# Kernel optimization log

Hardware: AMD Instinct MI355X
Metric: run time of the kernel (lower is better)

The kernel has to match this reference:

```python
import jax, jax.numpy as jnp
import numpy as np

B, N, T, F, H, NH, E, R = 16, 100, 96, 26, 128, 4, 16, 8


def _ln(x, g, b, eps=1e-5):
    m = x.mean(-1, keepdims=True)
    v = ((x - m) ** 2).mean(-1, keepdims=True)
    return (x - m) / jnp.sqrt(v + eps) * g + b


def setup_inputs() -> dict:
    ks = iter(jax.random.split(jax.random.key(0), 64))

    def nrm(*shape):
        return jax.random.normal(next(ks), shape, jnp.float32) * 0.05

    z = lambda *s: jnp.zeros(s, jnp.float32)
    o = lambda *s: jnp.ones(s, jnp.float32)
    inp = {}
    inp['x'] = jax.random.normal(next(ks), (B, N, T, F), jnp.float32)
    A = jax.random.uniform(next(ks), (N, N), jnp.float32)
    inp['A_norm'] = A / A.sum(1, keepdims=True)
    inp['H_inc'] = (jax.random.uniform(next(ks), (N, E)) > 0.7).astype(jnp.float32).at[:, 0].set(1.0)
    inp['membership'] = jax.random.randint(next(ks), (N,), 0, R)
    inp['Wp'] = nrm(H, F); inp['bp'] = z(H)
    inp['g_p'] = o(H); inp['b_p'] = z(H)
    inp['Wqkv'] = nrm(3 * H, H); inp['bqkv'] = z(3 * H)
    inp['Wo'] = nrm(H, H); inp['bo'] = z(H)
    inp['g_a'] = o(H); inp['b_a'] = z(H)
    inp['Wih_f'] = nrm(4 * H, H); inp['Whh_f'] = nrm(4 * H, H)
    inp['bih_f'] = z(4 * H); inp['bhh_f'] = z(4 * H)
    inp['Wih_b'] = nrm(4 * H, H); inp['Whh_b'] = nrm(4 * H, H)
    inp['bih_b'] = z(4 * H); inp['bhh_b'] = z(4 * H)
    inp['Wtp'] = nrm(H, 2 * H); inp['btp'] = z(H)
    inp['Wn'] = nrm(H, H); inp['bn'] = z(H)
    inp['We'] = nrm(H, H); inp['be'] = z(H)
    inp['Wa'] = nrm(1, H); inp['ba'] = z(1)
    inp['g_g'] = o(H); inp['b_g'] = z(H)
    inp['Remb'] = nrm(R, H)
    inp['Wg'] = nrm(H, H); inp['bg'] = z(H)
    inp['Wf'] = nrm(H, 2 * H); inp['bf'] = z(H)
    inp['g_f'] = o(H); inp['b_f'] = z(H)
    inp['W1'] = nrm(H // 2, H); inp['b1'] = z(H // 2)
    inp['W2'] = nrm(1, H // 2); inp['b2'] = z(1)
    return inp


def reference(x, A_norm, H_inc, membership, Wp, bp, g_p, b_p, Wqkv, bqkv, Wo, bo,
              g_a, b_a, Wih_f, Whh_f, bih_f, bhh_f, Wih_b, Whh_b, bih_b, bhh_b,
              Wtp, btp, Wn, bn, We, be, Wa, ba, g_g, b_g, Remb, Wg, bg,
              Wf, bf, g_f, b_f, W1, b1, W2, b2):
    B_, N_, T_, F_ = x.shape
    H_ = Wp.shape[0]
    BN = B_ * N_
    # input_proj (dropout = identity in eval)
    h = jax.nn.relu(_ln(x.reshape(BN, T_, F_) @ Wp.T + bp, g_p, b_p))
    # temporal multi-head self-attention + residual + LN
    qkv = h @ Wqkv.T + bqkv
    q, k, v = jnp.split(qkv, 3, -1)
    dh = H_ // NH
    sh = lambda t: t.reshape(BN, T_, NH, dh).transpose(0, 2, 1, 3)
    q, k, v = sh(q), sh(k), sh(v)
    att = jax.nn.softmax(jnp.einsum('bhqd,bhkd->bhqk', q, k) / jnp.sqrt(jnp.float32(dh)), -1)
    ao = jnp.einsum('bhqk,bhkd->bhqd', att, v).transpose(0, 2, 1, 3).reshape(BN, T_, H_)
    h = _ln(ao @ Wo.T + bo + h, g_a, b_a)
    # bidirectional LSTM (PyTorch gate order i,f,g,o), take t = T-1
    def lstm_scan(seq, Wih, Whh, bih, bhh):
        def step(carry, xt):
            hp, cp = carry
            gates = xt @ Wih.T + bih + hp @ Whh.T + bhh
            i, f, g, o_ = jnp.split(gates, 4, -1)
            c = jax.nn.sigmoid(f) * cp + jax.nn.sigmoid(i) * jnp.tanh(g)
            hn = jax.nn.sigmoid(o_) * jnp.tanh(c)
            return (hn, c), hn
        z0 = jnp.zeros((seq.shape[1], H_), seq.dtype)
        _, ys = jax.lax.scan(step, (z0, z0), seq)
        return ys
    seq = h.transpose(1, 0, 2)  # (T, BN, H)
    y_f = lstm_scan(seq, Wih_f, Whh_f, bih_f, bhh_f)[-1]        # fwd hidden at t=T-1
    y_b = lstm_scan(seq[::-1], Wih_b, Whh_b, bih_b, bhh_b)[0]   # bwd hidden at t=T-1
    h_temporal = (jnp.concatenate([y_f, y_b], -1) @ Wtp.T + btp).reshape(B_, N_, H_)
    # spatial: HyperGAT (segment softmax over incident hyperedges) + GCN + region emb
    mask = H_inc > 0                        # (N, E)
    deg_e = H_inc.sum(0)                    # (E,)
    has_edge = mask.any(-1, keepdims=True)  # (N, 1)
    r_emb = Remb[membership]                # (N, H)

    def spatial(hb):
        npj = hb @ Wn.T + bn
        ee = (H_inc.T @ npj) / (deg_e[:, None] + 1e-8)
        ee = ee @ We.T + be                 # (E, H)
        sc = (ee @ Wa.T + ba)[:, 0]         # (E,)
        w = jax.nn.softmax(jnp.where(mask, sc[None, :], -1e9), -1)
        w = jnp.where(has_edge, w, 0.0)
        hb2 = _ln(w @ ee + hb, g_g, b_g)
        hg = jax.nn.relu((A_norm @ hb2) @ Wg.T + bg)
        return hb2 + hg + r_emb

    h_spatial = jax.vmap(spatial)(h_temporal)
    h_fused = jax.nn.relu(_ln(jnp.concatenate([h_temporal, h_spatial], -1) @ Wf.T + bf, g_f, b_f))
    pred = (jax.nn.relu(h_fused @ W1.T + b1) @ W2.T + b2)[..., 0]
    return pred, h_spatial, h_temporal
```

## Files before the change

### kernel.cpp

```cpp
#include <hip/hip_runtime.h>
#include <hip/hip_bf16.h>

typedef __hip_bfloat16 bf16;
typedef __attribute__((ext_vector_type(8))) short bf8v;
typedef __attribute__((ext_vector_type(4))) short s4v;
typedef __attribute__((ext_vector_type(4))) float f4v;

#define DEV __device__ __forceinline__

DEV float b2f(bf16 v){ return __bfloat162float(v); }
DEV bf16 f2b(float v){ return __float2bfloat16(v); }
DEV short f2bs(float v){ bf16 t = __float2bfloat16(v); return *reinterpret_cast<short*>(&t); }
DEV float s2f(short s){ return __uint_as_float(((unsigned int)(unsigned short)s) << 16); }
DEV float blo(unsigned int u){ return __uint_as_float(u << 16); }
DEV float bhi(unsigned int u){ return __uint_as_float(u & 0xffff0000u); }
DEV float rcpf_(float x){ return __builtin_amdgcn_rcpf(x); }
DEV float sigf(float x){ return rcpf_(1.0f + __expf(-x)); }
DEV float tanhfast(float x){
  x = fminf(fmaxf(x, -15.0f), 15.0f);
  float e = __expf(-2.0f*x);
  return (1.0f - e)*rcpf_(1.0f + e);
}

DEV f4v mfma16(bf8v a, bf8v b, f4v c){
  return __builtin_amdgcn_mfma_f32_16x16x32_bf16(a, b, c, 0, 0, 0);
}

DEV float ln128(float s, int tid, const bf16* g, const bf16* b, float* red){
  float sum = s, sq = s*s;
  #pragma unroll
  for (int off = 32; off; off >>= 1){
    sum += __shfl_down(sum, off);
    sq  += __shfl_down(sq,  off);
  }
  if ((tid & 63) == 0){ red[(tid>>6)*2] = sum; red[(tid>>6)*2+1] = sq; }
  __syncthreads();
  float S = red[0] + red[2], Q = red[1] + red[3];
  float m  = S * (1.0f/128.0f);
  float var = fmaxf(Q * (1.0f/128.0f) - m*m, 0.0f);
  float rs = rsqrtf(var + 1e-5f);
  float y = (s - m)*rs*b2f(g[tid]) + b2f(b[tid]);
  __syncthreads();
  return y;
}

__global__ void k_detect(const unsigned int* __restrict__ xw, int* __restrict__ flag){
  __shared__ int found;
  if (threadIdx.x == 0) found = 0;
  __syncthreads();
  int local = 0;
  for (int i = threadIdx.x; i < 4096; i += 256){
    unsigned int u = xw[i];
    unsigned int e = (u >> 7) & 0xFF;
    if (e >= 0x90) local = 1;
  }
  if (local) atomicOr(&found, 1);
  __syncthreads();
  if (threadIdx.x == 0) flag[0] = found ? 0 : 1;
}

struct CArgs {
  const void* src[44];
  int n[44];
  int off[44];
};

__global__ void k_canon(CArgs a, const int* __restrict__ flag, bf16* __restrict__ dst){
  int id = blockIdx.y;
  int n = a.n[id];
  const void* s = a.src[id];
  bf16* d = dst + a.off[id];
  int stride = gridDim.x * blockDim.x;
  int i0 = blockIdx.x * blockDim.x + threadIdx.x;
  if (flag[0]){
    const bf16* sb = (const bf16*)s;
    for (int i = i0; i < n; i += stride) d[i] = sb[i];
  } else {
    const float* sf = (const float*)s;
    for (int i = i0; i < n; i += stride) d[i] = f2b(sf[i]);
  }
}

__global__ void k_inproj(const bf16* __restrict__ x, const bf16* __restrict__ Wp,
                         const bf16* __restrict__ bp, const bf16* __restrict__ gp,
                         const bf16* __restrict__ bbp, bf16* __restrict__ h0){
  int row0 = blockIdx.x*8, tid = threadIdx.x;
  __shared__ float xs[8*26];
  __shared__ float red[4];
  float wreg[26];
  #pragma unroll
  for (int f = 0; f < 26; ++f) wreg[f] = b2f(Wp[tid*26 + f]);
  float bias = b2f(bp[tid]);
  for (int i = tid; i < 208; i += 128) xs[i] = b2f(x[row0*26 + i]);
  __syncthreads();
  for (int r = 0; r < 8; ++r){
    float s = bias;
    #pragma unroll
    for (int f = 0; f < 26; ++f) s += xs[r*26 + f]*wreg[f];
    float y = fmaxf(ln128(s, tid, gp, bbp, red), 0.0f);
    h0[(row0 + r)*128 + tid] = f2b(y);
  }
}

__global__ __launch_bounds__(256) void k_attn(const bf16* __restrict__ h0,
    const bf16* __restrict__ Wqkv, const bf16* __restrict__ bqkv,
    bf16* __restrict__ attno){
  int bn = blockIdx.x;
  int tid = threadIdx.x;
  int w = tid >> 6;
  int lane = tid & 63;
  int l15 = lane & 15, quad = lane >> 4;

  __shared__ __align__(16) short h0s[96*136];
  __shared__ __align__(16) short v_sh[4][32*104];
  __shared__ __align__(16) short scr[4][16*40];

  {
    const uint4* src = (const uint4*)(h0 + bn*12288);
    uint4* dst = (uint4*)h0s;
    for (int u = tid; u < 1536; u += 256){
      int r = u >> 4, c = u & 15;
      dst[r*17 + c] = src[u];
    }
  }
  __syncthreads();

  short* vp = v_sh[w];
  short* sw = scr[w];
  const float scl = 0.17677669529663687f;

  bf8v aq[6], bk[6];
  for (int m = 0; m < 6; ++m){
    bf8v a[4];
    #pragma unroll
    for (int kt = 0; kt < 4; ++kt)
      a[kt] = *reinterpret_cast<const bf8v*>(h0s + (m*16 + l15)*136 + kt*32 + quad*8);
    #pragma unroll
    for (int n0 = 0; n0 < 32; n0 += 16){
      int rq = w*32 + n0 + l15;
      bf8v b[4];
      #pragma unroll
      for (int kt = 0; kt < 4; ++kt)
        b[kt] = *reinterpret_cast<const bf8v*>(Wqkv + rq*128 + kt*32 + quad*8);
      float bias = b2f(bqkv[rq]);
      f4v acc = {0.f,0.f,0.f,0.f};
      #pragma unroll
      for (int kt = 0; kt < 4; ++kt) acc = mfma16(a[kt], b[kt], acc);
      #pragma unroll
      for (int r = 0; r < 4; ++r)
        sw[(quad*4 + r)*40 + n0 + l15] = f2bs((acc[r] + bias)*scl);
    }
    asm volatile("s_waitcnt lgkmcnt(0)" ::: "memory");
    aq[m] = *reinterpret_cast<const bf8v*>(sw + l15*40 + quad*8);
  }
  for (int m = 0; m < 6; ++m){
    bf8v a[4];
    #pragma unroll
    for (int kt = 0; kt < 4; ++kt)
      a[kt] = *reinterpret_cast<const bf8v*>(h0s + (m*16 + l15)*136 + kt*32 + quad*8);
    #pragma unroll
    for (int n0 = 0; n0 < 32; n0 += 16){
      int rq = 128 + w*32 + n0 + l15;
      bf8v b[4];
      #pragma unroll
      for (int kt = 0; kt < 4; ++kt)
        b[kt] = *reinterpret_cast<const bf8v*>(Wqkv + rq*128 + kt*32 + quad*8);
      float bias = b2f(bqkv[rq]);
      f4v acc = {0.f,0.f,0.f,0.f};
      #pragma unroll
      for (int kt = 0; kt < 4; ++kt) acc = mfma16(a[kt], b[kt], acc);
      #pragma unroll
      for (int r = 0; r < 4; ++r)
        sw[(quad*4 + r)*40 + n0 + l15] = f2bs(acc[r] + bias);
    }
    asm volatile("s_waitcnt lgkmcnt(0)" ::: "memory");
    bk[m] = *reinterpret_cast<const bf8v*>(sw + l15*40 + quad*8);
  }
  for (int m = 0; m < 6; ++m){
    bf8v a[4];
    #pragma unroll
    for (int kt = 0; kt < 4; ++kt)
      a[kt] = *reinterpret_cast<const bf8v*>(h0s + (m*16 + l15)*136 + kt*32 + quad*8);
    #pragma unroll
// ... 86 lines not shown
    const uint4* src = (const uint4*)(attno + rt*16384);
    uint4* dst = (uint4*)atile;
    for (int u = tid; u < 2048; u += 256){
      int r = u >> 4, c = u & 15;
      dst[r*17 + c] = src[u];
    }
  }
  __syncthreads();
  int m0 = w*32;
  bf8v a[2][4];
  #pragma unroll
  for (int m = 0; m < 2; ++m)
    #pragma unroll
    for (int ksi = 0; ksi < 4; ++ksi)
      a[m][ksi] = *reinterpret_cast<const bf8v*>(atile + (m0 + m*16 + l15)*136 + ksi*32 + quad*8);
  f4v acc[2][8];
  #pragma unroll
  for (int m = 0; m < 2; ++m)
    #pragma unroll
    for (int n = 0; n < 8; ++n) acc[m][n] = (f4v){0.f,0.f,0.f,0.f};
  for (int n = 0; n < 8; ++n){
    int G = n*16 + l15;
    bf8v b[4];
    #pragma unroll
    for (int ksi = 0; ksi < 4; ++ksi)
      b[ksi] = *reinterpret_cast<const bf8v*>(Wo + G*128 + ksi*32 + quad*8);
    #pragma unroll
    for (int m = 0; m < 2; ++m)
      #pragma unroll
      for (int ksi = 0; ksi < 4; ++ksi)
        acc[m][n] = mfma16(a[m][ksi], b[ksi], acc[m][n]);
  }
  #pragma unroll
  for (int m = 0; m < 2; ++m){
    int rowbase = rt*128 + m0 + m*16;
    #pragma unroll
    for (int n = 0; n < 8; ++n){
      int col = n*16 + l15;
      float bia = b2f(bo[col]);
      #pragma unroll
      for (int r = 0; r < 4; ++r)
        acc[m][n][r] += bia + b2f(h0[(rowbase + quad*4 + r)*128 + col]);
    }
    float sm[4], sq[4];
    #pragma unroll
    for (int r = 0; r < 4; ++r){ sm[r] = 0.f; sq[r] = 0.f; }
    #pragma unroll
    for (int n = 0; n < 8; ++n)
      #pragma unroll
      for (int r = 0; r < 4; ++r){
        float v = acc[m][n][r];
        sm[r] += v; sq[r] += v*v;
      }
    #pragma unroll
    for (int mask = 1; mask < 16; mask <<= 1)
      #pragma unroll
      for (int r = 0; r < 4; ++r){
        sm[r] += __shfl_xor(sm[r], mask);
        sq[r] += __shfl_xor(sq[r], mask);
      }
    float mean[4], rs[4];
    #pragma unroll
    for (int r = 0; r < 4; ++r){
      mean[r] = sm[r]*(1.0f/128.0f);
      float var = fmaxf(sq[r]*(1.0f/128.0f) - mean[r]*mean[r], 0.0f);
      rs[r] = rsqrtf(var + 1e-5f);
    }
    #pragma unroll
    for (int n = 0; n < 8; ++n){
      int col = n*16 + l15;
      float gv = b2f(ga[col]), bv = b2f(ba_[col]);
      #pragma unroll
      for (int r = 0; r < 4; ++r){
        float y = (acc[m][n][r] - mean[r])*rs[r]*gv + bv;
        h1[(rowbase + quad*4 + r)*128 + col] = f2b(y);
      }
    }
  }
}

__global__ __launch_bounds__(512,1) void k_lstm(const bf16* __restrict__ Whh,
    const bf16* __restrict__ Wih, const bf16* __restrict__ bih,
    const bf16* __restrict__ bhh, const bf16* __restrict__ h1,
    float* __restrict__ y_f){
  int bn0 = blockIdx.x * 16;
  int tid = threadIdx.x;
  int w = tid >> 6, lane = tid & 63;
  int l15 = lane & 15, quad = lane >> 4;
  __shared__ __align__(16) short hbuf[2][16*136];
  __shared__ __align__(16) short xbuf[2][16*136];

  bf8v whh[4][4], wih[4][4];
  float bias[4];
  #pragma unroll
  for (int role = 0; role < 4; ++role){
    int G = role*128 + w*16 + l15;
    #pragma unroll
    for (int kt = 0; kt < 4; ++kt){
      whh[role][kt] = *reinterpret_cast<const bf8v*>(Whh + G*128 + kt*32 + quad*8);
      wih[role][kt] = *reinterpret_cast<const bf8v*>(Wih + G*128 + kt*32 + quad*8);
    }
    bias[role] = b2f(bih[G]) + b2f(bhh[G]);
  }
  const uint4* h1u4 = (const uint4*)h1;
  int srow = tid >> 4, scol = tid & 15;

  for (int i = tid; i < 16*136; i += 512) hbuf[0][i] = 0;
  if (tid < 256)
    ((uint4*)xbuf[0])[srow*17 + scol] = h1u4[((bn0 + srow)*96 + 0)*16 + scol];
  f4v c0 = {0.f,0.f,0.f,0.f};
  uint4 xpre;
  if (tid < 256) xpre = h1u4[((bn0 + srow)*96 + 1)*16 + scol];
  __syncthreads();

  f4v accx[4];
  {
    bf8v ax[4];
    #pragma unroll
    for (int kt = 0; kt < 4; ++kt)
      ax[kt] = *reinterpret_cast<const bf8v*>(xbuf[0] + l15*136 + kt*32 + quad*8);
    #pragma unroll
    for (int role = 0; role < 4; ++role){
      f4v z = {0.f,0.f,0.f,0.f};
      #pragma unroll
      for (int kt = 0; kt < 4; ++kt) z = mfma16(ax[kt], wih[role][kt], z);
      accx[role] = z;
    }
  }
  if (tid < 256) ((uint4*)xbuf[1])[srow*17 + scol] = xpre;
  if (tid < 256) xpre = h1u4[((bn0 + srow)*96 + 2)*16 + scol];
  __syncthreads();

  for (int t = 0; t < 96; ++t){
    int cur = t & 1, nxt = cur ^ 1;
    bf8v ah[4], axn[4];
    #pragma unroll
    for (int kt = 0; kt < 4; ++kt){
      ah[kt]  = *reinterpret_cast<const bf8v*>(hbuf[cur] + l15*136 + kt*32 + quad*8);
      axn[kt] = *reinterpret_cast<const bf8v*>(xbuf[nxt] + l15*136 + kt*32 + quad*8);
    }
    f4v acc[4];
    #pragma unroll
    for (int role = 0; role < 4; ++role){
      f4v z = accx[role];
      #pragma unroll
      for (int kt = 0; kt < 4; ++kt) z = mfma16(ah[kt], whh[role][kt], z);
      acc[role] = z;
    }
    #pragma unroll
    for (int role = 0; role < 4; ++role){
      f4v z = {0.f,0.f,0.f,0.f};
      #pragma unroll
      for (int kt = 0; kt < 4; ++kt) z = mfma16(axn[kt], wih[role][kt], z);
      accx[role] = z;
    }
    float hreg[4];
    #pragma unroll
    for (int r = 0; r < 4; ++r){
      float i_ = acc[0][r] + bias[0];
      float f_ = acc[1][r] + bias[1];
      float g_ = acc[2][r] + bias[2];
      float o_ = acc[3][r] + bias[3];
      float c  = sigf(f_)*c0[r] + sigf(i_)*tanhfast(g_);
      hreg[r]  = sigf(o_)*tanhfast(c);
      c0[r] = c;
    }
    #pragma unroll
    for (int r = 0; r < 4; ++r)
      hbuf[nxt][(quad*4 + r)*136 + w*16 + l15] = f2bs(hreg[r]);
    if (tid < 256){
      ((uint4*)xbuf[cur])[srow*17 + scol] = xpre;
      int tl = (t + 3 < 96) ? t + 3 : 95;
      xpre = h1u4[((bn0 + srow)*96 + tl)*16 + scol];
    }
    __syncthreads();
  }
  for (int idx = tid; idx < 2048; idx += 512){
    int r = idx >> 7, d = idx & 127;
    y_f[(bn0 + r)*128 + d] = s2f(hbuf[0][r*136 + d]);
  }
}

__global__ void k_bwdtp(const bf16* __restrict__ h1, const bf16* __restrict__ Wihb,
                        const bf16* __restrict__ bihb, const bf16* __restrict__ bhhb,
                        const float* __restrict__ y_f, const bf16* __restrict__ Wtp,
                        const bf16* __restrict__ btp, float* __restrict__ ht,
                        const int* __restrict__ flag, bf16* __restrict__ outb,
                        float* __restrict__ outf){
  int bn = blockIdx.x, tid = threadIdx.x;
  __shared__ __align__(16) float xr[128];
  __shared__ float gates[512];
  __shared__ __align__(16) float ycat[256];
  xr[tid] = b2f(h1[(bn*96 + 95)*128 + tid]);
  __syncthreads();
  const float2* xf2 = (const float2*)xr;
  for (int g = tid; g < 512; g += 128){
    const unsigned int* w = (const unsigned int*)(Wihb + g*128);
    float s = b2f(bihb[g]) + b2f(bhhb[g]);
    #pragma unroll 8
    for (int kp = 0; kp < 64; ++kp){
      float2 a = xf2[kp]; unsigned int u = w[kp];
      s += a.x*blo(u) + a.y*bhi(u);
    }
    gates[g] = s;
  }
  __syncthreads();
  float ii = gates[tid], gg = gates[256 + tid], oo = gates[384 + tid];
  float c  = sigf(ii)*tanhfast(gg);
  float yb = sigf(oo)*tanhfast(c);
  ycat[tid]       = y_f[bn*128 + tid];
  ycat[128 + tid] = yb;
  __syncthreads();
  const float2* yf2 = (const float2*)ycat;
  const unsigned int* w = (const unsigned int*)(Wtp + tid*256);
  float s = b2f(btp[tid]);
  #pragma unroll 8
  for (int kp = 0; kp < 128; ++kp){
    float2 a = yf2[kp]; unsigned int u = w[kp];
    s += a.x*blo(u) + a.y*bhi(u);
  }
  ht[bn*128 + tid] = s;
  int oi = 206400 + bn*128 + tid;
  if (flag[0]) outb[oi] = f2b(s); else outf[oi] = s;
}

__global__ void k_npj(const float* __restrict__ ht, const bf16* __restrict__ Wn,
                      const bf16* __restrict__ bn_, float* __restrict__ npj){
  int bn = blockIdx.x, tid = threadIdx.x;
  __shared__ __align__(16) float row[128];
  row[tid] = ht[bn*128 + tid];
  __syncthreads();
  const float2* rf2 = (const float2*)row;
  const unsigned int* w = (const unsigned int*)(Wn + tid*128);
  float s = b2f(bn_[tid]);
  #pragma unroll 8
  for (int kp = 0; kp < 64; ++kp){
    float2 a = rf2[kp]; unsigned int u = w[kp];
    s += a.x*blo(u) + a.y*bhi(u);
  }
  npj[bn*128 + tid] = s;
}

__global__ void k_edge(const float* __restrict__ npj, const bf16* __restrict__ Hinc,
                       const bf16* __restrict__ We, const bf16* __restrict__ be,
                       const bf16* __restrict__ Wa, const bf16* __restrict__ ba,
                       float* __restrict__ ee, float* __restrict__ scE){
  int b = blockIdx.x >> 4, e = blockIdx.x & 15, tid = threadIdx.x;
  float acc = 0.0f, deg = 0.0f;
  for (int n = 0; n < 100; ++n){
    float w = b2f(Hinc[n*16 + e]);
    deg += w;
    acc += w * npj[(b*100 + n)*128 + tid];
  }
  __shared__ __align__(16) float eep[128];
  eep[tid] = acc/(deg + 1e-8f);
  __syncthreads();
  const float2* ef2 = (const float2*)eep;
  const unsigned int* w = (const unsigned int*)(We + tid*128);
  float s = b2f(be[tid]);
  #pragma unroll 8
  for (int kp = 0; kp < 64; ++kp){
    float2 a = ef2[kp]; unsigned int u = w[kp];
    s += a.x*blo(u) + a.y*bhi(u);
  }
  ee[(b*16 + e)*128 + tid] = s;
  float p = s * b2f(Wa[tid]);
  #pragma unroll
  for (int off = 32; off; off >>= 1) p += __shfl_down(p, off);
  __shared__ float r2[2];
  if ((tid & 63) == 0) r2[tid>>6] = p;
  __syncthreads();
  if (tid == 0) scE[b*16 + e] = r2[0] + r2[1] + b2f(ba[0]);
}

__global__ void k_node(const float* __restrict__ ht, const float* __restrict__ ee,
                       const float* __restrict__ scE, const bf16* __restrict__ Hinc,
                       const bf16* __restrict__ gg_, const bf16* __restrict__ bg_,
                       float* __restrict__ hb2){
  int blk = blockIdx.x; int b = blk/100, n = blk%100; int tid = threadIdx.x;
  __shared__ float wts[16];
  __shared__ float red[4];
  if (tid == 0){
    float sc[16]; float mx = -1e30f;
    for (int e = 0; e < 16; ++e){
      float m_ = b2f(Hinc[n*16 + e]);
      sc[e] = (m_ > 0.0f) ? scE[b*16 + e] : -1e30f;
      mx = fmaxf(mx, sc[e]);
    }
    float tmp[16]; float sum = 0.0f;
    for (int e = 0; e < 16; ++e){
      tmp[e] = (sc[e] > -1e29f) ? __expf(sc[e] - mx) : 0.0f;
      sum += tmp[e];
    }
    float inv = (sum > 0.0f) ? 1.0f/sum : 0.0f;
    for (int e = 0; e < 16; ++e) wts[e] = tmp[e]*inv;
  }
  __syncthreads();
  float s = ht[(b*100 + n)*128 + tid];
  for (int e = 0; e < 16; ++e) s += wts[e] * ee[(b*16 + e)*128 + tid];
  float y = ln128(s, tid, gg_, bg_, red);
  hb2[(b*100 + n)*128 + tid] = y;
}

__global__ void k_gcn(const float* __restrict__ hb2, const bf16* __restrict__ An,
                      const bf16* __restrict__ Wg, const bf16* __restrict__ bg_,
                      const bf16* __restrict__ Remb, const int* __restrict__ mem,
                      float* __restrict__ hsp, const int* __restrict__ flag,
                      bf16* __restrict__ outb, float* __restrict__ outf){
  int blk = blockIdx.x; int b = blk/100, n = blk%100; int tid = threadIdx.x;
  float acc = 0.0f;
  for (int m = 0; m < 100; ++m){
    float a = b2f(An[n*100 + m]);
    acc += a * hb2[(b*100 + m)*128 + tid];
  }
  __shared__ __align__(16) float as_[128];
  as_[tid] = acc;
  __syncthreads();
  const float2* af2 = (const float2*)as_;
  const unsigned int* w = (const unsigned int*)(Wg + tid*128);
  float s = b2f(bg_[tid]);
  #pragma unroll 8
  for (int kp = 0; kp < 64; ++kp){
    float2 a = af2[kp]; unsigned int u = w[kp];
    s += a.x*blo(u) + a.y*bhi(u);
  }
  s = fmaxf(s, 0.0f);
  float out = hb2[(b*100 + n)*128 + tid] + s + b2f(Remb[mem[n]*128 + tid]);
  hsp[(b*100 + n)*128 + tid] = out;
  int oi = 1600 + (b*100 + n)*128 + tid;
  if (flag[0]) outb[oi] = f2b(out); else outf[oi] = out;
}

__global__ void k_fuse(const float* __restrict__ ht, const float* __restrict__ hsp,
                       const bf16* __restrict__ Wf, const bf16* __restrict__ bf_,
                       const bf16* __restrict__ gf, const bf16* __restrict__ b_f,
                       const bf16* __restrict__ W1, const bf16* __restrict__ b1,
                       const bf16* __restrict__ W2, const bf16* __restrict__ b2,
                       const int* __restrict__ flag, bf16* __restrict__ outb,
                       float* __restrict__ outf){
  int bn = blockIdx.x, tid = threadIdx.x;
  __shared__ __align__(16) float cat[256];
  __shared__ __align__(16) float hf[128];
  __shared__ float red[4];
  cat[tid]       = ht[bn*128 + tid];
  cat[128 + tid] = hsp[bn*128 + tid];
  __syncthreads();
  const float2* cf2 = (const float2*)cat;
  const unsigned int* w = (const unsigned int*)(Wf + tid*256);
  float s = b2f(bf_[tid]);
  #pragma unroll 8
  for (int kp = 0; kp < 128; ++kp){
    float2 a = cf2[kp]; unsigned int u = w[kp];
    s += a.x*blo(u) + a.y*bhi(u);
  }
  float y = fmaxf(ln128(s, tid, gf, b_f, red), 0.0f);
  hf[tid] = y;
  __syncthreads();
  if (tid < 64){
    const float2* hf2 = (const float2*)hf;
    const unsigned int* w1 = (const unsigned int*)(W1 + tid*128);
    float z = b2f(b1[tid]);
    #pragma unroll 8
    for (int kp = 0; kp < 64; ++kp){
      float2 a = hf2[kp]; unsigned int u = w1[kp];
      z += a.x*blo(u) + a.y*bhi(u);
    }
    z = fmaxf(z, 0.0f);
    float p = z * b2f(W2[tid]);
    #pragma unroll
    for (int off = 32; off; off >>= 1) p += __shfl_down(p, off);
    if (tid == 0){
      float pr = p + b2f(b2[0]);
      if (flag[0]) outb[bn] = f2b(pr); else outf[bn] = pr;
    }
  }
}


extern "C" void kernel_launch(void* const* d_in, const int* in_sizes, int n_in,
                              void* d_out, int out_size, void* d_ws, size_t ws_size,
                              hipStream_t stream){
  (void)n_in; (void)out_size; (void)ws_size;
  const int* mem = (const int*)d_in[3];

  CArgs ca;
  int coff[43];
  int nf = 0;
  long long off = 0;
  for (int i = 0; i < 43; ++i){
    if (i == 3){ coff[i] = -1; continue; }
    coff[i] = (int)off;
    ca.src[nf] = d_in[i];
    ca.n[nf]   = in_sizes[i];
    ca.off[nf] = (int)off;
    ++nf;
    off += (long long)((in_sizes[i] + 7) & ~7);
  }
  char* ws = (char*)d_ws;
  bf16* canon = (bf16*)ws;
  long long canonBytes = ((off*2 + 255)/256)*256;
  int* flag = (int*)(ws + canonBytes);
  long long base = canonBytes + 256;

  #define C(i) (canon + coff[i])
  const bf16* A_norm = C(1);
  const bf16* Hinc   = C(2);
  const bf16* Wp  = C(4);  const bf16* bp  = C(5);
  const bf16* g_p = C(6);  const bf16* b_p = C(7);
  const bf16* Wqkv= C(8);  const bf16* bqkv= C(9);
  const bf16* Wo  = C(10); const bf16* bo  = C(11);
  const bf16* g_a = C(12); const bf16* b_a = C(13);
  const bf16* Wih_f = C(14); const bf16* Whh_f = C(15);
  const bf16* bih_f = C(16); const bf16* bhh_f = C(17);
  const bf16* Wih_b = C(18);
  const bf16* bih_b = C(20); const bf16* bhh_b = C(21);
  const bf16* Wtp = C(22); const bf16* btp = C(23);
  const bf16* Wn  = C(24); const bf16* bn_ = C(25);
  const bf16* We  = C(26); const bf16* be  = C(27);
  const bf16* Wa  = C(28); const bf16* ba  = C(29);
  const bf16* g_g = C(30); const bf16* b_g = C(31);
  const bf16* Remb= C(32);
  const bf16* Wg  = C(33); const bf16* bg  = C(34);
  const bf16* Wf  = C(35); const bf16* bff = C(36);
  const bf16* g_f = C(37); const bf16* b_f = C(38);
  const bf16* W1  = C(39); const bf16* b1  = C(40);
  const bf16* W2  = C(41); const bf16* b2  = C(42);
  const bf16* xc  = C(0);
  #undef C

  bf16*  outb = (bf16*)d_out;
  float* outf = (float*)d_out;
  bf16*  h1    = (bf16*)(ws + base);
  bf16*  h0    = (bf16*)(ws + base + 39321600LL);
  bf16*  attno = (bf16*)(ws + base + 78643200LL);
  float* y_f   = (float*)(ws + base + 196608000LL);
  float* htb   = (float*)(ws + base + 197427200LL);
  float* npj   = (float*)(ws + base + 198246400LL);
  float* ee    = (float*)(ws + base + 199065600LL);
  float* scE   = (float*)(ws + base + 199196672LL);
  float* hb2   = (float*)(ws + base + 199197696LL);
  float* hsp   = (float*)(ws + base + 200016896LL);

  k_detect<<<1, 256, 0, stream>>>((const unsigned int*)d_in[0], flag);
  k_canon <<<dim3(64, nf), 256, 0, stream>>>(ca, flag, canon);
  k_inproj<<<19200, 128, 0, stream>>>(xc, Wp, bp, g_p, b_p, h0);
  k_attn  <<<1600,  256, 0, stream>>>(h0, Wqkv, bqkv, attno);
  k_oproj <<<1200,  256, 0, stream>>>(attno, h0, Wo, bo, g_a, b_a, h1);
  k_lstm  <<<100,   512, 0, stream>>>(Whh_f, Wih_f, bih_f, bhh_f, h1, y_f);
  k_bwdtp <<<1600,  128, 0, stream>>>(h1, Wih_b, bih_b, bhh_b, y_f, Wtp, btp, htb,
                                      flag, outb, outf);
  k_npj   <<<1600,  128, 0, stream>>>(htb, Wn, bn_, npj);
  k_edge  <<<256,   128, 0, stream>>>(npj, Hinc, We, be, Wa, ba, ee, scE);
  k_node  <<<1600,  128, 0, stream>>>(htb, ee, scE, Hinc, g_g, b_g, hb2);
  k_gcn   <<<1600,  128, 0, stream>>>(hb2, A_norm, Wg, bg, Remb, mem, hsp,
                                      flag, outb, outf);
  k_fuse  <<<1600,  128, 0, stream>>>(htb, hsp, Wf, bff, g_f, b_f, W1, b1, W2, b2,
                                      flag, outb, outf);
}
```

Baseline: 574.3 us.

## Move input projection to MFMA and fuse LSTM tail and spatial stages into few kernels

Replaces the scalar input-projection kernel with an MFMA tile version using a padded weight matrix and in-register layernorm. Folds the backward LSTM step and temporal projection into the tail of the forward LSTM kernel. Collapses the npj/edge/node/gcn/fuse chain into two per-batch kernels that use MFMA and shared memory. This cuts launch count and global round-trips and moves intermediates to bf16. The spatial kernels run only 16 blocks, so most of the GPU sits idle during those stages, and bf16 intermediates reduce precision.

```diff
diff --git a/kernel.cpp b/kernel.cpp
--- a/kernel.cpp
+++ b/kernel.cpp
@@ -12,8 +12,6 @@
 DEV bf16 f2b(float v){ return __float2bfloat16(v); }
 DEV short f2bs(float v){ bf16 t = __float2bfloat16(v); return *reinterpret_cast<short*>(&t); }
 DEV float s2f(short s){ return __uint_as_float(((unsigned int)(unsigned short)s) << 16); }
-DEV float blo(unsigned int u){ return __uint_as_float(u << 16); }
-DEV float bhi(unsigned int u){ return __uint_as_float(u & 0xffff0000u); }
 DEV float rcpf_(float x){ return __builtin_amdgcn_rcpf(x); }
 DEV float sigf(float x){ return rcpf_(1.0f + __expf(-x)); }
 DEV float tanhfast(float x){
@@ -24,24 +22,6 @@
 
 DEV f4v mfma16(bf8v a, bf8v b, f4v c){
   return __builtin_amdgcn_mfma_f32_16x16x32_bf16(a, b, c, 0, 0, 0);
-}
-
-DEV float ln128(float s, int tid, const bf16* g, const bf16* b, float* red){
-  float sum = s, sq = s*s;
-  #pragma unroll
-  for (int off = 32; off; off >>= 1){
-    sum += __shfl_down(sum, off);
-    sq  += __shfl_down(sq,  off);
-  }
-  if ((tid & 63) == 0){ red[(tid>>6)*2] = sum; red[(tid>>6)*2+1] = sq; }
-  __syncthreads();
-  float S = red[0] + red[2], Q = red[1] + red[3];
-  float m  = S * (1.0f/128.0f);
-  float var = fmaxf(Q * (1.0f/128.0f) - m*m, 0.0f);
-  float rs = rsqrtf(var + 1e-5f);
-  float y = (s - m)*rs*b2f(g[tid]) + b2f(b[tid]);
-  __syncthreads();
-  return y;
 }
 
 __global__ void k_detect(const unsigned int* __restrict__ xw, int* __restrict__ flag){
@@ -81,24 +61,101 @@
   }
 }
 
-__global__ void k_inproj(const bf16* __restrict__ x, const bf16* __restrict__ Wp,
-                         const bf16* __restrict__ bp, const bf16* __restrict__ gp,
-                         const bf16* __restrict__ bbp, bf16* __restrict__ h0){
-  int row0 = blockIdx.x*8, tid = threadIdx.x;
-  __shared__ float xs[8*26];
-  __shared__ float red[4];
-  float wreg[26];
+__global__ void k_prep(const bf16* __restrict__ Wp, const bf16* __restrict__ An,
+                       bf16* __restrict__ Wpp, bf16* __restrict__ Anp,
+                       bf16* __restrict__ htp, bf16* __restrict__ hb2p){
+  int stride = gridDim.x * blockDim.x;
+  bf16 zero = f2b(0.0f);
+  for (int i = blockIdx.x*blockDim.x + threadIdx.x; i < 477184; i += stride){
+    if (i < 4096){
+      int row = i >> 5, col = i & 31;
+      Wpp[i] = (col < 26) ? Wp[row*26 + col] : zero;
+    } else if (i < 18432){
+      int j = i - 4096;
+      int row = j >> 7, col = j & 127;
+      Anp[j] = (row < 100 && col < 100) ? An[row*100 + col] : zero;
+    } else if (i < 247808){
+      htp[i - 18432] = zero;
+    } else {
+      hb2p[i - 247808] = zero;
+    }
+  }
+}
+
+__global__ __launch_bounds__(256) void k_inproj(const bf16* __restrict__ x,
+    const bf16* __restrict__ Wpp, const bf16* __restrict__ bp,
+    const bf16* __restrict__ gp, const bf16* __restrict__ bbp,
+    bf16* __restrict__ h0){
+  int blk = blockIdx.x, tid = threadIdx.x;
+  int w = tid >> 6, lane = tid & 63, l15 = lane & 15, quad = lane >> 4;
+  __shared__ __align__(16) short flat[3328];
+  __shared__ __align__(16) short xt[128*40];
+  {
+    const uint4* src = (const uint4*)(x + blk*3328);
+    uint4* dst = (uint4*)flat;
+    for (int u = tid; u < 416; u += 256) dst[u] = src[u];
+  }
+  __syncthreads();
+  for (int i = tid; i < 5120; i += 256){
+    int row = i/40, col = i - row*40;
+    xt[i] = (col < 26) ? flat[row*26 + col] : (short)0;
+  }
+  __syncthreads();
+  int m0 = w*32;
+  bf8v a[2];
   #pragma unroll
-  for (int f = 0; f < 26; ++f) wreg[f] = b2f(Wp[tid*26 + f]);
-  float bias = b2f(bp[tid]);
-  for (int i = tid; i < 208; i += 128) xs[i] = b2f(x[row0*26 + i]);
-  __syncthreads();
-  for (int r = 0; r < 8; ++r){
-    float s = bias;
-    #pragma unroll
-    for (int f = 0; f < 26; ++f) s += xs[r*26 + f]*wreg[f];
-    float y = fmaxf(ln128(s, tid, gp, bbp, red), 0.0f);
-    h0[(row0 + r)*128 + tid] = f2b(y);
+  for (int m = 0; m < 2; ++m)
+    a[m] = *reinterpret_cast<const bf8v*>(xt + (m0 + m*16 + l15)*40 + quad*8);
+  f4v acc[2][8];
+  for (int n = 0; n < 8; ++n){
+    bf8v bb = *reinterpret_cast<const bf8v*>(Wpp + (n*16 + l15)*32 + quad*8);
+    #pragma unroll
+    for (int m = 0; m < 2; ++m){
+      f4v z = {0.f,0.f,0.f,0.f};
+      acc[m][n] = mfma16(a[m], bb, z);
+    }
+  }
+  #pragma unroll
+  for (int m = 0; m < 2; ++m){
+    int rowbase = blk*128 + m0 + m*16;
+    float sm[4], sq[4];
+    #pragma unroll
+    for (int r = 0; r < 4; ++r){ sm[r] = 0.f; sq[r] = 0.f; }
+    #pragma unroll
+    for (int n = 0; n < 8; ++n){
+      int col = n*16 + l15;
+      float bv = b2f(bp[col]);
+      #pragma unroll
+      for (int r = 0; r < 4; ++r){
+        float v = acc[m][n][r] + bv;
+        acc[m][n][r] = v;
+        sm[r] += v; sq[r] += v*v;
+      }
+    }
+    #pragma unroll
+    for (int mask = 1; mask < 16; mask <<= 1)
+      #pragma unroll
+      for (int r = 0; r < 4; ++r){
+        sm[r] += __shfl_xor(sm[r], mask);
+        sq[r] += __shfl_xor(sq[r], mask);
+      }
+    float mean[4], rs[4];
+    #pragma unroll
+    for (int r = 0; r < 4; ++r){
+      mean[r] = sm[r]*(1.0f/128.0f);
+      float var = fmaxf(sq[r]*(1.0f/128.0f) - mean[r]*mean[r], 0.0f);
+      rs[r] = rsqrtf(var + 1e-5f);
+    }
+    #pragma unroll
+    for (int n = 0; n < 8; ++n){
+      int col = n*16 + l15;
+      float gv = b2f(gp[col]), bv = b2f(bbp[col]);
+      #pragma unroll
+      for (int r = 0; r < 4; ++r){
+        float y = fmaxf((acc[m][n][r] - mean[r])*rs[r]*gv + bv, 0.0f);
+        h0[(rowbase + quad*4 + r)*128 + col] = f2b(y);
+      }
+    }
   }
 }
 
@@ -351,13 +408,18 @@
 __global__ __launch_bounds__(512,1) void k_lstm(const bf16* __restrict__ Whh,
     const bf16* __restrict__ Wih, const bf16* __restrict__ bih,
     const bf16* __restrict__ bhh, const bf16* __restrict__ h1,
-    float* __restrict__ y_f){
+    const bf16* __restrict__ Wihb, const bf16* __restrict__ bihb,
+    const bf16* __restrict__ bhhb, const bf16* __restrict__ Wtp,
+    const bf16* __restrict__ btp, bf16* __restrict__ ht_pad,
+    const int* __restrict__ flag, bf16* __restrict__ outb,
+    float* __restrict__ outf){
   int bn0 = blockIdx.x * 16;
   int tid = threadIdx.x;
   int w = tid >> 6, lane = tid & 63;
   int l15 = lane & 15, quad = lane >> 4;
   __shared__ __align__(16) short hbuf[2][16*136];
   __shared__ __align__(16) short xbuf[2][16*136];
+  __shared__ __align__(16) short ycat[16*264];
 
   bf8v whh[4][4], wih[4][4];
   float bias[4];
@@ -446,202 +508,331 @@
   }
   for (int idx = tid; idx < 2048; idx += 512){
     int r = idx >> 7, d = idx & 127;
-    y_f[(bn0 + r)*128 + d] = s2f(hbuf[0][r*136 + d]);
-  }
-}
-
-__global__ void k_bwdtp(const bf16* __restrict__ h1, const bf16* __restrict__ Wihb,
-                        const bf16* __restrict__ bihb, const bf16* __restrict__ bhhb,
-                        const float* __restrict__ y_f, const bf16* __restrict__ Wtp,
-                        const bf16* __restrict__ btp, float* __restrict__ ht,
-                        const int* __restrict__ flag, bf16* __restrict__ outb,
-                        float* __restrict__ outf){
-  int bn = blockIdx.x, tid = threadIdx.x;
-  __shared__ __align__(16) float xr[128];
-  __shared__ float gates[512];
-  __shared__ __align__(16) float ycat[256];
-  xr[tid] = b2f(h1[(bn*96 + 95)*128 + tid]);
-  __syncthreads();
-  const float2* xf2 = (const float2*)xr;
-  for (int g = tid; g < 512; g += 128){
-    const unsigned int* w = (const unsigned int*)(Wihb + g*128);
-    float s = b2f(bihb[g]) + b2f(bhhb[g]);
-    #pragma unroll 8
-    for (int kp = 0; kp < 64; ++kp){
-      float2 a = xf2[kp]; unsigned int u = w[kp];
-      s += a.x*blo(u) + a.y*bhi(u);
-    }
-    gates[g] = s;
-  }
-  __syncthreads();
-  float ii = gates[tid], gg = gates[256 + tid], oo = gates[384 + tid];
-  float c  = sigf(ii)*tanhfast(gg);
-  float yb = sigf(oo)*tanhfast(c);
-  ycat[tid]       = y_f[bn*128 + tid];
-  ycat[128 + tid] = yb;
-  __syncthreads();
-  const float2* yf2 = (const float2*)ycat;
-  const unsigned int* w = (const unsigned int*)(Wtp + tid*256);
-  float s = b2f(btp[tid]);
-  #pragma unroll 8
-  for (int kp = 0; kp < 128; ++kp){
-    float2 a = yf2[kp]; unsigned int u = w[kp];
-    s += a.x*blo(u) + a.y*bhi(u);
-  }
-  ht[bn*128 + tid] = s;
-  int oi = 206400 + bn*128 + tid;
-  if (flag[0]) outb[oi] = f2b(s); else outf[oi] = s;
-}
-
-__global__ void k_npj(const float* __restrict__ ht, const bf16* __restrict__ Wn,
-                      const bf16* __restrict__ bn_, float* __restrict__ npj){
-  int bn = blockIdx.x, tid = threadIdx.x;
-  __shared__ __align__(16) float row[128];
-  row[tid] = ht[bn*128 + tid];
-  __syncthreads();
-  const float2* rf2 = (const float2*)row;
-  const unsigned int* w = (const unsigned int*)(Wn + tid*128);
-  float s = b2f(bn_[tid]);
-  #pragma unroll 8
-  for (int kp = 0; kp < 64; ++kp){
-    float2 a = rf2[kp]; unsigned int u = w[kp];
-    s += a.x*blo(u) + a.y*bhi(u);
-  }
-  npj[bn*128 + tid] = s;
-}
-
-__global__ void k_edge(const float* __restrict__ npj, const bf16* __restrict__ Hinc,
-                       const bf16* __restrict__ We, const bf16* __restrict__ be,
-                       const bf16* __restrict__ Wa, const bf16* __restrict__ ba,
-                       float* __restrict__ ee, float* __restrict__ scE){
-  int b = blockIdx.x >> 4, e = blockIdx.x & 15, tid = threadIdx.x;
-  float acc = 0.0f, deg = 0.0f;
-  for (int n = 0; n < 100; ++n){
-    float w = b2f(Hinc[n*16 + e]);
-    deg += w;
-    acc += w * npj[(b*100 + n)*128 + tid];
-  }
-  __shared__ __align__(16) float eep[128];
-  eep[tid] = acc/(deg + 1e-8f);
-  __syncthreads();
-  const float2* ef2 = (const float2*)eep;
-  const unsigned int* w = (const unsigned int*)(We + tid*128);
-  float s = b2f(be[tid]);
-  #pragma unroll 8
-  for (int kp = 0; kp < 64; ++kp){
-    float2 a = ef2[kp]; unsigned int u = w[kp];
-    s += a.x*blo(u) + a.y*bhi(u);
-  }
-  ee[(b*16 + e)*128 + tid] = s;
-  float p = s * b2f(Wa[tid]);
-  #pragma unroll
-  for (int off = 32; off; off >>= 1) p += __shfl_down(p, off);
-  __shared__ float r2[2];
-  if ((tid & 63) == 0) r2[tid>>6] = p;
-  __syncthreads();
-  if (tid == 0) scE[b*16 + e] = r2[0] + r2[1] + b2f(ba[0]);
-}
-
-__global__ void k_node(const float* __restrict__ ht, const float* __restrict__ ee,
-                       const float* __restrict__ scE, const bf16* __restrict__ Hinc,
-                       const bf16* __restrict__ gg_, const bf16* __restrict__ bg_,
-                       float* __restrict__ hb2){
-  int blk = blockIdx.x; int b = blk/100, n = blk%100; int tid = threadIdx.x;
-  __shared__ float wts[16];
-  __shared__ float red[4];
-  if (tid == 0){
-    float sc[16]; float mx = -1e30f;
+    ycat[r*264 + d] = hbuf[0][r*136 + d];
+  }
+  {
+    bf8v ax[4];
+    #pragma unroll
+    for (int kt = 0; kt < 4; ++kt)
+      ax[kt] = *reinterpret_cast<const bf8v*>(xbuf[0] + l15*136 + kt*32 + quad*8);
+    int col = w*16 + l15;
+    f4v gi = {0.f,0.f,0.f,0.f}, gg = {0.f,0.f,0.f,0.f}, go = {0.f,0.f,0.f,0.f};
+    #pragma unroll
+    for (int kt = 0; kt < 4; ++kt){
+      gi = mfma16(ax[kt], *reinterpret_cast<const bf8v*>(Wihb + col*128 + kt*32 + quad*8), gi);
+      gg = mfma16(ax[kt], *reinterpret_cast<const bf8v*>(Wihb + (256 + col)*128 + kt*32 + quad*8), gg);
+      go = mfma16(ax[kt], *reinterpret_cast<const bf8v*>(Wihb + (384 + col)*128 + kt*32 + quad*8), go);
+    }
+    float bi = b2f(bihb[col])       + b2f(bhhb[col]);
+    float bg = b2f(bihb[256 + col]) + b2f(bhhb[256 + col]);
+    float bo = b2f(bihb[384 + col]) + b2f(bhhb[384 + col]);
+    #pragma unroll
+    for (int r = 0; r < 4; ++r){
+      float c  = sigf(gi[r] + bi) * tanhfast(gg[r] + bg);
+      float yb = sigf(go[r] + bo) * tanhfast(c);
+      ycat[(quad*4 + r)*264 + 128 + col] = f2bs(yb);
+    }
+  }
+  __syncthreads();
+  {
+    int col = w*16 + l15;
+    f4v z = {0.f,0.f,0.f,0.f};
+    #pragma unroll
+    for (int kt = 0; kt < 8; ++kt){
+      bf8v a = *reinterpret_cast<const bf8v*>(ycat + l15*264 + kt*32 + quad*8);
+      bf8v bb = *reinterpret_cast<const bf8v*>(Wtp + col*256 + kt*32 + quad*8);
+      z = mfma16(a, bb, z);
+    }
+    float bt = b2f(btp[col]);
+    #pragma unroll
+    for (int r = 0; r < 4; ++r){
+      int rowg = bn0 + quad*4 + r;
+      float v = z[r] + bt;
+      int bb_ = rowg/100, nn = rowg - bb_*100;
+      ht_pad[(bb_*112 + nn)*128 + col] = f2b(v);
+      int oi = 206400 + rowg*128 + col;
+      if (flag[0]) outb[oi] = f2b(v); else outf[oi] = v;
+    }
+  }
+}
+
+__global__ __launch_bounds__(512,1) void k_spat1(
+    const bf16* __restrict__ ht_pad, const bf16* __restrict__ Hinc,
+    const bf16* __restrict__ Wn, const bf16* __restrict__ bn_,
+    const bf16* __restrict__ We, const bf16* __restrict__ be,
+    const bf16* __restrict__ Wa, const bf16* __restrict__ ba,
+    const bf16* __restrict__ gg_, const bf16* __restrict__ bg_,
+    bf16* __restrict__ hb2g){
+  int b = blockIdx.x, tid = threadIdx.x;
+  int w = tid >> 6, lane = tid & 63, l15 = lane & 15, quad = lane >> 4;
+  __shared__ __align__(16) short htb[112*136];
+  __shared__ __align__(16) short mtile[16*136];
+  __shared__ float HincS[1600];
+  __shared__ float wts[1600];
+  __shared__ float eeS[16*128];
+  __shared__ float scE[16], degS[16], part[128];
+
+  {
+    const uint4* src = (const uint4*)(ht_pad + b*14336);
+    uint4* dst = (uint4*)htb;
+    for (int u = tid; u < 1792; u += 512){
+      int r = u >> 4, c = u & 15;
+      dst[r*17 + c] = src[u];
+    }
+  }
+  for (int i = tid; i < 1600; i += 512) HincS[i] = b2f(Hinc[i]);
+  __syncthreads();
+  if (tid < 16){
+    float s = 0.0f;
+    for (int n = 0; n < 100; ++n) s += HincS[n*16 + tid];
+    degS[tid] = s;
+  }
+  __syncthreads();
+  for (int it = 0; it < 4; ++it){
+    int idx = tid + it*512;
+    int e = idx >> 7, d = idx & 127;
+    float s = 0.0f;
+    for (int n = 0; n < 100; ++n)
+      s += HincS[n*16 + e] * s2f(htb[n*136 + d]);
+    mtile[e*136 + d] = f2bs(s * rcpf_(degS[e] + 1e-8f));
+  }
+  __syncthreads();
+  {
+    bf8v a[4];
+    #pragma unroll
+    for (int kt = 0; kt < 4; ++kt)
+      a[kt] = *reinterpret_cast<const bf8v*>(mtile + l15*136 + kt*32 + quad*8);
+    int col = w*16 + l15;
+    f4v z = {0.f,0.f,0.f,0.f};
+    #pragma unroll
+    for (int kt = 0; kt < 4; ++kt)
+      z = mfma16(a[kt], *reinterpret_cast<const bf8v*>(Wn + col*128 + kt*32 + quad*8), z);
+    float bnv = b2f(bn_[col]);
+    __syncthreads();
+    #pragma unroll
+    for (int r = 0; r < 4; ++r){
+      int e = quad*4 + r;
+      float ratio = degS[e] * rcpf_(degS[e] + 1e-8f);
+      mtile[e*136 + col] = f2bs(z[r] + bnv*ratio);
+    }
+  }
+  __syncthreads();
+  {
+    bf8v a[4];
+    #pragma unroll
+    for (int kt = 0; kt < 4; ++kt)
+      a[kt] = *reinterpret_cast<const bf8v*>(mtile + l15*136 + kt*32 + quad*8);
+    int col = w*16 + l15;
+    f4v z = {0.f,0.f,0.f,0.f};
+    #pragma unroll
+    for (int kt = 0; kt < 4; ++kt)
+      z = mfma16(a[kt], *reinterpret_cast<const bf8v*>(We + col*128 + kt*32 + quad*8), z);
+    float bev = b2f(be[col]);
+    #pragma unroll
+    for (int r = 0; r < 4; ++r)
+      eeS[(quad*4 + r)*128 + col] = z[r] + bev;
+  }
+  __syncthreads();
+  if (tid < 128){
+    int e = tid >> 3, j = tid & 7;
+    float s = 0.0f;
+    for (int d = j*16; d < j*16 + 16; ++d)
+      s += eeS[e*128 + d] * b2f(Wa[d]);
+    part[tid] = s;
+  }
+  __syncthreads();
+  if (tid < 16){
+    float s = b2f(ba[0]);
+    for (int j = 0; j < 8; ++j) s += part[tid*8 + j];
+    scE[tid] = s;
+  }
+  __syncthreads();
+  if (tid < 100){
+    float sc[16], mx = -1e30f;
     for (int e = 0; e < 16; ++e){
-      float m_ = b2f(Hinc[n*16 + e]);
-      sc[e] = (m_ > 0.0f) ? scE[b*16 + e] : -1e30f;
+      sc[e] = (HincS[tid*16 + e] > 0.0f) ? scE[e] : -1e30f;
       mx = fmaxf(mx, sc[e]);
     }
-    float tmp[16]; float sum = 0.0f;
+    float sum = 0.0f, tmp[16];
     for (int e = 0; e < 16; ++e){
       tmp[e] = (sc[e] > -1e29f) ? __expf(sc[e] - mx) : 0.0f;
       sum += tmp[e];
     }
-    float inv = (sum > 0.0f) ? 1.0f/sum : 0.0f;
-    for (int e = 0; e < 16; ++e) wts[e] = tmp[e]*inv;
-  }
-  __syncthreads();
-  float s = ht[(b*100 + n)*128 + tid];
-  for (int e = 0; e < 16; ++e) s += wts[e] * ee[(b*16 + e)*128 + tid];
-  float y = ln128(s, tid, gg_, bg_, red);
-  hb2[(b*100 + n)*128 + tid] = y;
-}
-
-__global__ void k_gcn(const float* __restrict__ hb2, const bf16* __restrict__ An,
-                      const bf16* __restrict__ Wg, const bf16* __restrict__ bg_,
-                      const bf16* __restrict__ Remb, const int* __restrict__ mem,
-                      float* __restrict__ hsp, const int* __restrict__ flag,
-                      bf16* __restrict__ outb, float* __restrict__ outf){
-  int blk = blockIdx.x; int b = blk/100, n = blk%100; int tid = threadIdx.x;
-  float acc = 0.0f;
-  for (int m = 0; m < 100; ++m){
-    float a = b2f(An[n*100 + m]);
-    acc += a * hb2[(b*100 + m)*128 + tid];
-  }
-  __shared__ __align__(16) float as_[128];
-  as_[tid] = acc;
-  __syncthreads();
-  const float2* af2 = (const float2*)as_;
-  const unsigned int* w = (const unsigned int*)(Wg + tid*128);
-  float s = b2f(bg_[tid]);
-  #pragma unroll 8
-  for (int kp = 0; kp < 64; ++kp){
-    float2 a = af2[kp]; unsigned int u = w[kp];
-    s += a.x*blo(u) + a.y*bhi(u);
-  }
-  s = fmaxf(s, 0.0f);
-  float out = hb2[(b*100 + n)*128 + tid] + s + b2f(Remb[mem[n]*128 + tid]);
-  hsp[(b*100 + n)*128 + tid] = out;
-  int oi = 1600 + (b*100 + n)*128 + tid;
-  if (flag[0]) outb[oi] = f2b(out); else outf[oi] = out;
-}
-
-__global__ void k_fuse(const float* __restrict__ ht, const float* __restrict__ hsp,
-                       const bf16* __restrict__ Wf, const bf16* __restrict__ bf_,
-                       const bf16* __restrict__ gf, const bf16* __restrict__ b_f,
-                       const bf16* __restrict__ W1, const bf16* __restrict__ b1,
-                       const bf16* __restrict__ W2, const bf16* __restrict__ b2,
-                       const int* __restrict__ flag, bf16* __restrict__ outb,
-                       float* __restrict__ outf){
-  int bn = blockIdx.x, tid = threadIdx.x;
-  __shared__ __align__(16) float cat[256];
-  __shared__ __align__(16) float hf[128];
-  __shared__ float red[4];
-  cat[tid]       = ht[bn*128 + tid];
-  cat[128 + tid] = hsp[bn*128 + tid];
-  __syncthreads();
-  const float2* cf2 = (const float2*)cat;
-  const unsigned int* w = (const unsigned int*)(Wf + tid*256);
-  float s = b2f(bf_[tid]);
-  #pragma unroll 8
-  for (int kp = 0; kp < 128; ++kp){
-    float2 a = cf2[kp]; unsigned int u = w[kp];
-    s += a.x*blo(u) + a.y*bhi(u);
-  }
-  float y = fmaxf(ln128(s, tid, gf, b_f, red), 0.0f);
-  hf[tid] = y;
-  __syncthreads();
-  if (tid < 64){
-    const float2* hf2 = (const float2*)hf;
-    const unsigned int* w1 = (const unsigned int*)(W1 + tid*128);
-    float z = b2f(b1[tid]);
-    #pragma unroll 8
-    for (int kp = 0; kp < 64; ++kp){
-      float2 a = hf2[kp]; unsigned int u = w1[kp];
-      z += a.x*blo(u) + a.y*bhi(u);
-    }
-    z = fmaxf(z, 0.0f);
-    float p = z * b2f(W2[tid]);
-    #pragma unroll
-    for (int off = 32; off; off >>= 1) p += __shfl_down(p, off);
-    if (tid == 0){
-      float pr = p + b2f(b2[0]);
-      if (flag[0]) outb[bn] = f2b(pr); else outf[bn] = pr;
-    }
+    float inv = (sum > 0.0f) ? rcpf_(sum) : 0.0f;
+    for (int e = 0; e < 16; ++e) wts[tid*16 + e] = tmp[e]*inv;
+  }
+  __syncthreads();
+  for (int it = 0; it < 13; ++it){
+    int n = it*8 + w;
+    if (n < 100){
+      int d0 = lane*2;
+      float s0 = s2f(htb[n*136 + d0]);
+      float s1 = s2f(htb[n*136 + d0 + 1]);
+      for (int e = 0; e < 16; ++e){
+        float wv = wts[n*16 + e];
+        s0 += wv * eeS[e*128 + d0];
+        s1 += wv * eeS[e*128 + d0 + 1];
+      }
+      float sum = s0 + s1, sq = s0*s0 + s1*s1;
+      #pragma unroll
+      for (int mask = 1; mask < 64; mask <<= 1){
+        sum += __shfl_xor(sum, mask);
+        sq  += __shfl_xor(sq, mask);
+      }
+      float mean = sum*(1.0f/128.0f);
+      float var = fmaxf(sq*(1.0f/128.0f) - mean*mean, 0.0f);
+      float rs = rsqrtf(var + 1e-5f);
+      float y0 = (s0 - mean)*rs*b2f(gg_[d0])     + b2f(bg_[d0]);
+      float y1 = (s1 - mean)*rs*b2f(gg_[d0 + 1]) + b2f(bg_[d0 + 1]);
+      hb2g[b*14336 + n*128 + d0]     = f2b(y0);
+      hb2g[b*14336 + n*128 + d0 + 1] = f2b(y1);
+    }
+  }
+}
+
+__global__ __launch_bounds__(512,1) void k_spat2(
+    const bf16* __restrict__ hb2g, const bf16* __restrict__ Anp,
+    const bf16* __restrict__ Wg, const bf16* __restrict__ bgc,
+    const bf16* __restrict__ Remb, const int* __restrict__ mem,
+    const bf16* __restrict__ ht_pad,
+    const bf16* __restrict__ Wf, const bf16* __restrict__ bf_,
+    const bf16* __restrict__ gf, const bf16* __restrict__ b_f,
+    const bf16* __restrict__ W1, const bf16* __restrict__ b1,
+    const bf16* __restrict__ W2, const bf16* __restrict__ b2,
+    const int* __restrict__ flag, bf16* __restrict__ outb,
+    float* __restrict__ outf){
+  int b = blockIdx.x, tid = threadIdx.x;
+  int w = tid >> 6, lane = tid & 63, l15 = lane & 15, quad = lane >> 4;
+  __shared__ __align__(16) short regA[128*136];
+  __shared__ __align__(16) short regB[112*136];
+
+  for (int i = tid; i < 128*136; i += 512) regA[i] = 0;
+  __syncthreads();
+  {
+    int c0 = w*16;
+    bf8v bw[4];
+    #pragma unroll
+    for (int kt = 0; kt < 4; ++kt)
+      bw[kt] = *reinterpret_cast<const bf8v*>(Wg + (c0 + l15)*128 + kt*32 + quad*8);
+    for (int m = 0; m < 7; ++m){
+      f4v z = {0.f,0.f,0.f,0.f};
+      #pragma unroll
+      for (int kt = 0; kt < 4; ++kt){
+        bf8v a = *reinterpret_cast<const bf8v*>(hb2g + b*14336 + (m*16 + l15)*128 + kt*32 + quad*8);
+        z = mfma16(a, bw[kt], z);
+      }
+      s4v vs;
+      #pragma unroll
+      for (int r = 0; r < 4; ++r) vs[r] = f2bs(z[r]);
+      *reinterpret_cast<s4v*>(regA + (c0 + l15)*136 + m*16 + quad*4) = vs;
+    }
+  }
+  __syncthreads();
+  {
+    int c0 = w*16;
+    for (int m = 0; m < 7; ++m){
+      f4v z = {0.f,0.f,0.f,0.f};
+      #pragma unroll
+      for (int kt = 0; kt < 4; ++kt){
+        bf8v a  = *reinterpret_cast<const bf8v*>(Anp + (m*16 + l15)*128 + kt*32 + quad*8);
+        bf8v bb = *reinterpret_cast<const bf8v*>(regA + (c0 + l15)*136 + kt*32 + quad*8);
+        z = mfma16(a, bb, z);
+      }
+      #pragma unroll
+      for (int r = 0; r < 4; ++r){
+        int row = m*16 + quad*4 + r, col = c0 + l15;
+        if (row < 100){
+          float v = fmaxf(z[r] + b2f(bgc[col]), 0.0f);
+          float o = b2f(hb2g[b*14336 + row*128 + col]) + v
+                  + b2f(Remb[mem[row]*128 + col]);
+          int oi = 1600 + (b*100 + row)*128 + col;
+          if (flag[0]) outb[oi] = f2b(o); else outf[oi] = o;
+          regB[row*136 + col] = f2bs(o);
+        } else {
+          regB[row*136 + col] = 0;
+        }
+      }
+    }
+  }
+  __syncthreads();
+  if (w < 7){
+    int m = w;
+    f4v acc[8];
+    for (int n = 0; n < 8; ++n){
+      f4v z = {0.f,0.f,0.f,0.f};
+      #pragma unroll
+      for (int kt = 0; kt < 4; ++kt){
+        bf8v a  = *reinterpret_cast<const bf8v*>(ht_pad + b*14336 + (m*16 + l15)*128 + kt*32 + quad*8);
+        bf8v bb = *reinterpret_cast<const bf8v*>(Wf + (n*16 + l15)*256 + kt*32 + quad*8);
+        z = mfma16(a, bb, z);
+      }
+      #pragma unroll
+      for (int kt = 0; kt < 4; ++kt){
+        bf8v a  = *reinterpret_cast<const bf8v*>(regB + (m*16 + l15)*136 + kt*32 + quad*8);
+        bf8v bb = *reinterpret_cast<const bf8v*>(Wf + (n*16 + l15)*256 + 128 + kt*32 + quad*8);
+        z = mfma16(a, bb, z);
+      }
+      acc[n] = z;
+    }
+    float sm[4], sq[4];
+    #pragma unroll
+    for (int r = 0; r < 4; ++r){ sm[r] = 0.f; sq[r] = 0.f; }
+    #pragma unroll
+    for (int n = 0; n < 8; ++n){
+      int col = n*16 + l15;
+      float bv = b2f(bf_[col]);
+      #pragma unroll
+      for (int r = 0; r < 4; ++r){
+        float v = acc[n][r] + bv;
+        acc[n][r] = v;
+        sm[r] += v; sq[r] += v*v;
+      }
+    }
+    #pragma unroll
+    for (int mask = 1; mask < 16; mask <<= 1)
+      #pragma unroll
+      for (int r = 0; r < 4; ++r){
+        sm[r] += __shfl_xor(sm[r], mask);
+        sq[r] += __shfl_xor(sq[r], mask);
+      }
+    #pragma unroll
+    for (int r = 0; r < 4; ++r){
+      float mean = sm[r]*(1.0f/128.0f);
+      float var = fmaxf(sq[r]*(1.0f/128.0f) - mean*mean, 0.0f);
+      float rs = rsqrtf(var + 1e-5f);
+      #pragma unroll
+      for (int n = 0; n < 8; ++n){
+        int col = n*16 + l15;
+        float y = fmaxf((acc[n][r] - mean)*rs*b2f(gf[col]) + b2f(b_f[col]), 0.0f);
+        regA[(m*16 + quad*4 + r)*136 + col] = f2bs(y);
+      }
+    }
+  }
+  __syncthreads();
+  if (w < 7){
+    int m = w;
+    for (int n = 0; n < 4; ++n){
+      f4v z = {0.f,0.f,0.f,0.f};
+      #pragma unroll
+      for (int kt = 0; kt < 4; ++kt){
+        bf8v a  = *reinterpret_cast<const bf8v*>(regA + (m*16 + l15)*136 + kt*32 + quad*8);
+        bf8v bb = *reinterpret_cast<const bf8v*>(W1 + (n*16 + l15)*128 + kt*32 + quad*8);
+        z = mfma16(a, bb, z);
+      }
+      #pragma unroll
+      for (int r = 0; r < 4; ++r){
+        int row = m*16 + quad*4 + r, col = n*16 + l15;
+        regB[row*72 + col] = f2bs(fmaxf(z[r] + b2f(b1[col]), 0.0f));
+      }
+    }
+  }
+  __syncthreads();
+  if (tid < 100){
+    float s = b2f(b2[0]);
+    for (int d = 0; d < 64; ++d)
+      s += s2f(regB[tid*72 + d]) * b2f(W2[d]);
+    int oi = b*100 + tid;
+    if (flag[0]) outb[oi] = f2b(s); else outf[oi] = s;
   }
 }
 
@@ -699,30 +890,26 @@
 
   bf16*  outb = (bf16*)d_out;
   float* outf = (float*)d_out;
-  bf16*  h1    = (bf16*)(ws + base);
-  bf16*  h0    = (bf16*)(ws + base + 39321600LL);
-  bf16*  attno = (bf16*)(ws + base + 78643200LL);
-  float* y_f   = (float*)(ws + base + 196608000LL);
-  float* htb   = (float*)(ws + base + 197427200LL);
-  float* npj   = (float*)(ws + base + 198246400LL);
-  float* ee    = (float*)(ws + base + 199065600LL);
-  float* scE   = (float*)(ws + base + 199196672LL);
-  float* hb2   = (float*)(ws + base + 199197696LL);
-  float* hsp   = (float*)(ws + base + 200016896LL);
+  bf16*  h1     = (bf16*)(ws + base);
+  bf16*  h0     = (bf16*)(ws + base + 39321600LL);
+  bf16*  attno  = (bf16*)(ws + base + 78643200LL);
+  bf16*  Wpp    = (bf16*)(ws + base + 196608000LL);
+  bf16*  An_pad = (bf16*)(ws + base + 196616192LL);
+  bf16*  ht_pad = (bf16*)(ws + base + 196644864LL);
+  bf16*  hb2g   = (bf16*)(ws + base + 197103616LL);
 
   k_detect<<<1, 256, 0, stream>>>((const unsigned int*)d_in[0], flag);
   k_canon <<<dim3(64, nf), 256, 0, stream>>>(ca, flag, canon);
-  k_inproj<<<19200, 128, 0, stream>>>(xc, Wp, bp, g_p, b_p, h0);
-  k_attn  <<<1600,  256, 0, stream>>>(h0, Wqkv, bqkv, attno);
-  k_oproj <<<1200,  256, 0, stream>>>(attno, h0, Wo, bo, g_a, b_a, h1);
-  k_lstm  <<<100,   512, 0, stream>>>(Whh_f, Wih_f, bih_f, bhh_f, h1, y_f);
-  k_bwdtp <<<1600,  128, 0, stream>>>(h1, Wih_b, bih_b, bhh_b, y_f, Wtp, btp, htb,
-                                      flag, outb, outf);
-  k_npj   <<<1600,  128, 0, stream>>>(htb, Wn, bn_, npj);
-  k_edge  <<<256,   128, 0, stream>>>(npj, Hinc, We, be, Wa, ba, ee, scE);
-  k_node  <<<1600,  128, 0, stream>>>(htb, ee, scE, Hinc, g_g, b_g, hb2);
-  k_gcn   <<<1600,  128, 0, stream>>>(hb2, A_norm, Wg, bg, Remb, mem, hsp,
-                                      flag, outb, outf);
-  k_fuse  <<<1600,  128, 0, stream>>>(htb, hsp, Wf, bff, g_f, b_f, W1, b1, W2, b2,
-                                      flag, outb, outf);
-}
+  k_prep  <<<1024, 256, 0, stream>>>(Wp, A_norm, Wpp, An_pad, ht_pad, hb2g);
+  k_inproj<<<1200, 256, 0, stream>>>(xc, Wpp, bp, g_p, b_p, h0);
+  k_attn  <<<1600, 256, 0, stream>>>(h0, Wqkv, bqkv, attno);
+  k_oproj <<<1200, 256, 0, stream>>>(attno, h0, Wo, bo, g_a, b_a, h1);
+  k_lstm  <<<100,  512, 0, stream>>>(Whh_f, Wih_f, bih_f, bhh_f, h1,
+                                     Wih_b, bih_b, bhh_b, Wtp, btp, ht_pad,
+                                     flag, outb, outf);
+  k_spat1 <<<16,   512, 0, stream>>>(ht_pad, Hinc, Wn, bn_, We, be, Wa, ba,
+                                     g_g, b_g, hb2g);
+  k_spat2 <<<16,   512, 0, stream>>>(hb2g, An_pad, Wg, bg, Remb, mem, ht_pad,
+                                     Wf, bff, g_f, b_f, W1, b1, W2, b2,
+                                     flag, outb, outf);
+}
```

After: 514.7 us. 10.4% less time.
